# Kernel tuning notes

Measured on AMD Instinct MI355X. Metric: run time of the kernel, lower is better.

The kernel has to match this reference:

```python
import jax, jax.numpy as jnp
import numpy as np

B, T, M, S = 16384, 128, 4, 12  # num_series, timesteps, measurements, states


def setup_inputs() -> dict:
    key = jax.random.key(0)
    ks = jax.random.split(key, 7)
    inp = jax.random.normal(ks[0], (B, T, M), dtype=jnp.float32)
    # stable transition matrix near identity
    F = jnp.eye(S, dtype=jnp.float32) + 0.05 * jax.random.normal(ks[1], (S, S), dtype=jnp.float32) / np.float32(np.sqrt(S))
    H = jax.random.normal(ks[2], (M, S), dtype=jnp.float32) / np.float32(np.sqrt(S))
    Aq = 0.1 * jax.random.normal(ks[3], (S, S), dtype=jnp.float32)
    Q = Aq @ Aq.T + 1e-3 * jnp.eye(S, dtype=jnp.float32)  # PSD process noise
    Ar = 0.1 * jax.random.normal(ks[4], (M, M), dtype=jnp.float32)
    R = Ar @ Ar.T + 1e-3 * jnp.eye(M, dtype=jnp.float32)  # PSD measurement noise
    m0 = jax.random.normal(ks[5], (B, S, 1), dtype=jnp.float32)
    Ap = 0.1 * jax.random.normal(ks[6], (B, S, S), dtype=jnp.float32)
    P0 = jnp.einsum('bij,bkj->bik', Ap, Ap) + 1e-2 * jnp.eye(S, dtype=jnp.float32)
    return {"inp": inp, "F": F, "H": H, "Q": Q, "R": R, "m0": m0, "P0": P0}


def _kalman_forward(inp, F, H, Q, R, m0, P0):
    I_S = jnp.eye(S, dtype=inp.dtype)
    # t = -1 step of the original loop: one predict from the initial state
    m = jnp.einsum('ij,bjk->bik', F, m0)                      # [B,S,1]
    P = jnp.einsum('ij,bjk,lk->bil', F, P0, F) + Q            # [B,S,S]

    def step(carry, obs_t):
        m, P = carry  # one-step-ahead prior at time t
        y = jnp.einsum('ms,bsk->bmk', H, m)                   # predicted measurement [B,M,1]
        # --- kf_update ---
        resid = obs_t - y[..., 0]                             # [B,M]
        Sm = jnp.einsum('ms,bst,nt->bmn', H, P, H) + R        # innovation cov [B,M,M]
        Sinv = jnp.linalg.inv(Sm)
        K = jnp.einsum('bst,mt,bmn->bsn', P, H, Sinv)         # Kalman gain [B,S,M]
        m_f = m + jnp.einsum('bsm,bm->bs', K, resid)[..., None]
        ImKH = I_S - jnp.einsum('bsm,mt->bst', K, H)
        # Joseph stabilized covariance update
        P_f = (jnp.einsum('bij,bjk,blk->bil', ImKH, P, ImKH)
               + jnp.einsum('bim,mn,bjn->bij', K, R, K))
        # --- kf_predict for next timestep ---
        m_n = jnp.einsum('ij,bjk->bik', F, m_f)
        P_n = jnp.einsum('ij,bjk,lk->bil', F, P_f, F) + Q
        return (m_n, P_n), y

    _, ys = jax.lax.scan(step, (m, P), jnp.swapaxes(inp, 0, 1))  # ys: [T,B,M,1]
    # original forward does torch.cat(predicted_measurements, 0) -> [T*B, M, 1]
    return ys.reshape(T * B, M, 1)


def reference(inp, F, H, Q, R, m0, P0):
    return _kalman_forward(inp, F, H, Q, R, m0, P0)
```

## Files before the change

### kernel.cpp

```cpp
#include <hip/hip_runtime.h>

#define BN 16384
#define TT 128
#define MM 4
#define SS 12
#define BLOCK 64
#define NSER (BLOCK / 4)
#define TSTRIDE 145


template<int CTRL>
__device__ __forceinline__ float dpp32(float v) {
    union { int i; float f; } u, o;
    u.f = v;
    o.i = __builtin_amdgcn_update_dpp(0, u.i, CTRL, 0xF, 0xF, true);
    return o.f;
}
template<int CTRL>
__device__ __forceinline__ double dpp64(double v) {
    union { double d; int i[2]; } u, o;
    u.d = v;
    o.i[0] = __builtin_amdgcn_update_dpp(0, u.i[0], CTRL, 0xF, 0xF, true);
    o.i[1] = __builtin_amdgcn_update_dpp(0, u.i[1], CTRL, 0xF, 0xF, true);
    return o.d;
}
__device__ __forceinline__ double qsum(double v) {
    v += dpp64<0xB1>(v);
    v += dpp64<0x4E>(v);
    return v;
}

__global__ __launch_bounds__(BLOCK, 1) void kf_kernel(
    const float* __restrict__ inp,
    const float* __restrict__ Fm,
    const float* __restrict__ Hm,
    const float* __restrict__ Qm,
    const float* __restrict__ Rm,
    const float* __restrict__ m0p,
    const float* __restrict__ P0p,
    float* __restrict__ outp)
{
    __shared__ double Fd[SS * SS];
    __shared__ double Hd[MM * SS];
    __shared__ double Qd[SS * SS];
    __shared__ double Rd[MM * MM];
    __shared__ double tb[NSER * TSTRIDE];

    const int tid  = threadIdx.x;
    const int gid  = blockIdx.x * BLOCK + tid;
    const int b    = gid >> 2;
    const int c    = gid & 3;
    const int sb   = tid >> 2;
    const int col0 = 3 * c;

    for (int i = tid; i < SS * SS; i += BLOCK) {
        Fd[i] = (double)Fm[i];
        Qd[i] = (double)Qm[i];
    }
    if (tid < MM * SS) Hd[tid] = (double)Hm[tid];
    if (tid < MM * MM) Rd[tid] = (double)Rm[tid];

    double P[SS][3];
#pragma unroll
    for (int s = 0; s < SS; ++s)
#pragma unroll
        for (int jj = 0; jj < 3; ++jj)
            P[s][jj] = (double)P0p[b * SS * SS + s * SS + col0 + jj];

    double mtmp[SS];
#pragma unroll
    for (int s = 0; s < SS; ++s) mtmp[s] = (double)m0p[b * SS + s];

    const float* op = inp + b * (TT * MM) + c;
    float obn = op[0];
    double* tser = &tb[sb * TSTRIDE];

    __syncthreads();

#pragma unroll
    for (int i = 0; i < SS; ++i) {
        double fr[SS];
#pragma unroll
        for (int s = 0; s < SS; ++s) fr[s] = Fd[i * SS + s];
        double u0 = 0.0, u1 = 0.0, u2 = 0.0;
#pragma unroll
        for (int s = 0; s < SS; ++s) {
            u0 += fr[s] * P[s][0];
            u1 += fr[s] * P[s][1];
            u2 += fr[s] * P[s][2];
        }
        tser[i * SS + col0 + 0] = u0;
        tser[i * SS + col0 + 1] = u1;
        tser[i * SS + col0 + 2] = u2;
    }
    double pmv[3];
#pragma unroll
    for (int jj = 0; jj < 3; ++jj) {
        double a = 0.0;
#pragma unroll
        for (int s = 0; s < SS; ++s) a += Fd[(col0 + jj) * SS + s] * mtmp[s];
        pmv[jj] = a;
    }
    __builtin_amdgcn_wave_barrier();
#pragma unroll
    for (int h = 0; h < 2; ++h) {
        double Ur[3][6];
#pragma unroll
        for (int jj = 0; jj < 3; ++jj)
#pragma unroll
            for (int kk = 0; kk < 6; ++kk)
                Ur[jj][kk] = tser[(col0 + jj) * SS + h * 6 + kk];
#pragma unroll
        for (int s = 0; s < SS; ++s) {
            double fr6[6];
#pragma unroll
            for (int kk = 0; kk < 6; ++kk) fr6[kk] = Fd[s * SS + h * 6 + kk];
            double p0 = (h == 0) ? Qd[s * SS + col0 + 0] : P[s][0];
            double p1 = (h == 0) ? Qd[s * SS + col0 + 1] : P[s][1];
            double p2 = (h == 0) ? Qd[s * SS + col0 + 2] : P[s][2];
#pragma unroll
            for (int kk = 0; kk < 6; ++kk) {
                p0 += Ur[0][kk] * fr6[kk];
                p1 += Ur[1][kk] * fr6[kk];
                p2 += Ur[2][kk] * fr6[kk];
            }
            P[s][0] = p0; P[s][1] = p1; P[s][2] = p2;
        }
    }
    double mvf[SS];
    mvf[0]  = dpp64<0x00>(pmv[0]);  mvf[1]  = dpp64<0x00>(pmv[1]);  mvf[2]  = dpp64<0x00>(pmv[2]);
    mvf[3]  = dpp64<0x55>(pmv[0]);  mvf[4]  = dpp64<0x55>(pmv[1]);  mvf[5]  = dpp64<0x55>(pmv[2]);
    mvf[6]  = dpp64<0xAA>(pmv[0]);  mvf[7]  = dpp64<0xAA>(pmv[1]);  mvf[8]  = dpp64<0xAA>(pmv[2]);
    mvf[9]  = dpp64<0xFF>(pmv[0]);  mvf[10] = dpp64<0xFF>(pmv[1]);  mvf[11] = dpp64<0xFF>(pmv[2]);

#pragma unroll 1
    for (int t = 0; t < TT; ++t) {
        __builtin_amdgcn_wave_barrier();

#pragma unroll
        for (int i = 0; i < SS; ++i) {
            double fr[SS];
#pragma unroll
            for (int s = 0; s < SS; ++s) fr[s] = Fd[i * SS + s];
            double u0 = 0.0, u1 = 0.0, u2 = 0.0;
#pragma unroll
            for (int s = 0; s < SS; ++s) {
                u0 += fr[s] * P[s][0];
                u1 += fr[s] * P[s][1];
                u2 += fr[s] * P[s][2];
            }
            tser[i * SS + col0 + 0] = u0;
            tser[i * SS + col0 + 1] = u1;
            tser[i * SS + col0 + 2] = u2;
        }

        double fmv[3];
#pragma unroll
        for (int jj = 0; jj < 3; ++jj) {
            double a = 0.0;
#pragma unroll
            for (int s = 0; s < SS; ++s) a += Fd[(col0 + jj) * SS + s] * mvf[s];
            fmv[jj] = a;
        }

        double y[MM];
#pragma unroll
        for (int n = 0; n < MM; ++n) {
            double py = Hd[n * SS + col0 + 0] * mvf[col0 + 0]
                      + Hd[n * SS + col0 + 1] * mvf[col0 + 1]
                      + Hd[n * SS + col0 + 2] * mvf[col0 + 2];
            y[n] = qsum(py);
        }
        double ysel = (c & 2) ? ((c & 1) ? y[3] : y[2]) : ((c & 1) ? y[1] : y[0]);
        outp[t * (BN * MM) + b * MM + c] = (float)ysel;

        float obc = obn;
        if (t + 1 < TT) obn = op[(t + 1) * MM];

        double r[MM];
        r[0] = (double)dpp32<0x00>(obc) - y[0];
        r[1] = (double)dpp32<0x55>(obc) - y[1];
        r[2] = (double)dpp32<0xAA>(obc) - y[2];
        r[3] = (double)dpp32<0xFF>(obc) - y[3];

        double HPl[MM][3];
#pragma unroll
        for (int n = 0; n < MM; ++n) {
            double h0 = 0.0, h1 = 0.0, h2 = 0.0;
#pragma unroll
            for (int s = 0; s < SS; ++s) {
                double hv = Hd[n * SS + s];
                h0 += hv * P[s][0]; h1 += hv * P[s][1]; h2 += hv * P[s][2];
            }
            HPl[n][0] = h0; HPl[n][1] = h1; HPl[n][2] = h2;
        }

        double Su[10];
        {
            int u = 0;
#pragma unroll
            for (int n = 0; n < MM; ++n)
#pragma unroll
                for (int t2 = 0; t2 < MM; ++t2) {
                    if (t2 < n) continue;
                    double acc = HPl[n][0] * Hd[t2 * SS + col0 + 0]
                               + HPl[n][1] * Hd[t2 * SS + col0 + 1]
                               + HPl[n][2] * Hd[t2 * SS + col0 + 2];
                    Su[u] = qsum(acc) + Rd[n * MM + t2];
                    ++u;
                }
        }
        double s00 = Su[0], s01 = Su[1], s02 = Su[2], s03 = Su[3];
        double s11 = Su[4], s12 = Su[5], s13 = Su[6];
        double s22 = Su[7], s23 = Su[8], s33 = Su[9];

        __builtin_amdgcn_wave_barrier();

#pragma unroll
        for (int h = 0; h < 2; ++h) {
            double Ur[3][6];
#pragma unroll
            for (int jj = 0; jj < 3; ++jj)
#pragma unroll
                for (int kk = 0; kk < 6; ++kk)
                    Ur[jj][kk] = tser[(col0 + jj) * SS + h * 6 + kk];
#pragma unroll
            for (int s = 0; s < SS; ++s) {
                double fr6[6];
#pragma unroll
                for (int kk = 0; kk < 6; ++kk) fr6[kk] = Fd[s * SS + h * 6 + kk];
                double p0 = (h == 0) ? Qd[s * SS + col0 + 0] : P[s][0];
                double p1 = (h == 0) ? Qd[s * SS + col0 + 1] : P[s][1];
                double p2 = (h == 0) ? Qd[s * SS + col0 + 2] : P[s][2];
#pragma unroll
                for (int kk = 0; kk < 6; ++kk) {
                    p0 += Ur[0][kk] * fr6[kk];
                    p1 += Ur[1][kk] * fr6[kk];
                    p2 += Ur[2][kk] * fr6[kk];
                }
                P[s][0] = p0; P[s][1] = p1; P[s][2] = p2;
            }
        }

        double Vl[MM][3];
        {
            double h00 = dpp64<0x00>(HPl[0][0]), h01 = dpp64<0x00>(HPl[0][1]), h02 = dpp64<0x00>(HPl[0][2]);
            double h10 = dpp64<0x00>(HPl[1][0]), h11 = dpp64<0x00>(HPl[1][1]), h12 = dpp64<0x00>(HPl[1][2]);
            double h20 = dpp64<0x00>(HPl[2][0]), h21 = dpp64<0x00>(HPl[2][1]), h22 = dpp64<0x00>(HPl[2][2]);
            double h30 = dpp64<0x00>(HPl[3][0]), h31 = dpp64<0x00>(HPl[3][1]), h32 = dpp64<0x00>(HPl[3][2]);
#pragma unroll
            for (int jj = 0; jj < 3; ++jj) {
                double f0 = Fd[(col0 + jj) * SS + 0], f1 = Fd[(col0 + jj) * SS + 1], f2 = Fd[(col0 + jj) * SS + 2];
                Vl[0][jj] = h00 * f0 + h01 * f1 + h02 * f2;
                Vl[1][jj] = h10 * f0 + h11 * f1 + h12 * f2;
                Vl[2][jj] = h20 * f0 + h21 * f1 + h22 * f2;
                Vl[3][jj] = h30 * f0 + h31 * f1 + h32 * f2;
            }
        }
        {
            double h00 = dpp64<0x55>(HPl[0][0]), h01 = dpp64<0x55>(HPl[0][1]), h02 = dpp64<0x55>(HPl[0][2]);
            double h10 = dpp64<0x55>(HPl[1][0]), h11 = dpp64<0x55>(HPl[1][1]), h12 = dpp64<0x55>(HPl[1][2]);
            double h20 = dpp64<0x55>(HPl[2][0]), h21 = dpp64<0x55>(HPl[2][1]), h22 = dpp64<0x55>(HPl[2][2]);
            double h30 = dpp64<0x55>(HPl[3][0]), h31 = dpp64<0x55>(HPl[3][1]), h32 = dpp64<0x55>(HPl[3][2]);
#pragma unroll
            for (int jj = 0; jj < 3; ++jj) {
                double f0 = Fd[(col0 + jj) * SS + 3], f1 = Fd[(col0 + jj) * SS + 4], f2 = Fd[(col0 + jj) * SS + 5];
                Vl[0][jj] += h00 * f0 + h01 * f1 + h02 * f2;
                Vl[1][jj] += h10 * f0 + h11 * f1 + h12 * f2;
                Vl[2][jj] += h20 * f0 + h21 * f1 + h22 * f2;
                Vl[3][jj] += h30 * f0 + h31 * f1 + h32 * f2;
            }
        }
        {
            double h00 = dpp64<0xAA>(HPl[0][0]), h01 = dpp64<0xAA>(HPl[0][1]), h02 = dpp64<0xAA>(HPl[0][2]);
            double h10 = dpp64<0xAA>(HPl[1][0]), h11 = dpp64<0xAA>(HPl[1][1]), h12 = dpp64<0xAA>(HPl[1][2]);
            double h20 = dpp64<0xAA>(HPl[2][0]), h21 = dpp64<0xAA>(HPl[2][1]), h22 = dpp64<0xAA>(HPl[2][2]);
            double h30 = dpp64<0xAA>(HPl[3][0]), h31 = dpp64<0xAA>(HPl[3][1]), h32 = dpp64<0xAA>(HPl[3][2]);
#pragma unroll
            for (int jj = 0; jj < 3; ++jj) {
                double f0 = Fd[(col0 + jj) * SS + 6], f1 = Fd[(col0 + jj) * SS + 7], f2 = Fd[(col0 + jj) * SS + 8];
                Vl[0][jj] += h00 * f0 + h01 * f1 + h02 * f2;
                Vl[1][jj] += h10 * f0 + h11 * f1 + h12 * f2;
                Vl[2][jj] += h20 * f0 + h21 * f1 + h22 * f2;
                Vl[3][jj] += h30 * f0 + h31 * f1 + h32 * f2;
            }
        }
        {
            double h00 = dpp64<0xFF>(HPl[0][0]), h01 = dpp64<0xFF>(HPl[0][1]), h02 = dpp64<0xFF>(HPl[0][2]);
            double h10 = dpp64<0xFF>(HPl[1][0]), h11 = dpp64<0xFF>(HPl[1][1]), h12 = dpp64<0xFF>(HPl[1][2]);
            double h20 = dpp64<0xFF>(HPl[2][0]), h21 = dpp64<0xFF>(HPl[2][1]), h22 = dpp64<0xFF>(HPl[2][2]);
            double h30 = dpp64<0xFF>(HPl[3][0]), h31 = dpp64<0xFF>(HPl[3][1]), h32 = dpp64<0xFF>(HPl[3][2]);
#pragma unroll
            for (int jj = 0; jj < 3; ++jj) {
                double f0 = Fd[(col0 + jj) * SS + 9], f1 = Fd[(col0 + jj) * SS + 10], f2 = Fd[(col0 + jj) * SS + 11];
                Vl[0][jj] += h00 * f0 + h01 * f1 + h02 * f2;
                Vl[1][jj] += h10 * f0 + h11 * f1 + h12 * f2;
                Vl[2][jj] += h20 * f0 + h21 * f1 + h22 * f2;
                Vl[3][jj] += h30 * f0 + h31 * f1 + h32 * f2;
            }
        }

        double ra   = 1.0 / (s00 * s11 - s01 * s01);
        double ai00 = s11 * ra, ai01 = -s01 * ra, ai11 = s00 * ra;
        double w00 = ai00 * s02 + ai01 * s12;
        double w01 = ai00 * s03 + ai01 * s13;
        double w10 = ai01 * s02 + ai11 * s12;
        double w11 = ai01 * s03 + ai11 * s13;
        double e00 = s22 - (s02 * w00 + s12 * w10);
        double e01 = s23 - (s02 * w01 + s12 * w11);
        double e11 = s33 - (s03 * w01 + s13 * w11);
        double rmm = 1.0 / (e00 * e11 - e01 * e01);
        double q22 = e11 * rmm, q23 = -e01 * rmm, q33 = e00 * rmm;
        double x00 = w00 * q22 + w01 * q23;
        double x01 = w00 * q23 + w01 * q33;
        double x10 = w10 * q22 + w11 * q23;
        double x11 = w10 * q23 + w11 * q33;
        double q00 = ai00 + x00 * w00 + x01 * w01;
        double q01 = ai01 + x00 * w10 + x01 * w11;
        double q11 = ai11 + x10 * w10 + x11 * w11;
        double Qi[MM][MM] = {
            { q00,  q01,  -x00, -x01 },
            { q01,  q11,  -x10, -x11 },
            { -x00, -x10,  q22,  q23 },
            { -x01, -x11,  q23,  q33 }
        };

        double z0 = Qi[0][0] * r[0] + Qi[0][1] * r[1] + Qi[0][2] * r[2] + Qi[0][3] * r[3];
        double z1 = Qi[1][0] * r[0] + Qi[1][1] * r[1] + Qi[1][2] * r[2] + Qi[1][3] * r[3];
        double z2 = Qi[2][0] * r[0] + Qi[2][1] * r[1] + Qi[2][2] * r[2] + Qi[2][3] * r[3];
        double z3 = Qi[3][0] * r[0] + Qi[3][1] * r[1] + Qi[3][2] * r[2] + Qi[3][3] * r[3];

        double G2[MM][3];
#pragma unroll
        for (int n = 0; n < MM; ++n)
#pragma unroll
            for (int jj = 0; jj < 3; ++jj)
                G2[n][jj] = Qi[n][0] * Vl[0][jj] + Qi[n][1] * Vl[1][jj]
                          + Qi[n][2] * Vl[2][jj] + Qi[n][3] * Vl[3][jj];

        {
            double v00 = dpp64<0x00>(Vl[0][0]), v01 = dpp64<0x00>(Vl[0][1]), v02 = dpp64<0x00>(Vl[0][2]);
            double v10 = dpp64<0x00>(Vl[1][0]), v11 = dpp64<0x00>(Vl[1][1]), v12 = dpp64<0x00>(Vl[1][2]);
            double v20 = dpp64<0x00>(Vl[2][0]), v21 = dpp64<0x00>(Vl[2][1]), v22 = dpp64<0x00>(Vl[2][2]);
            double v30 = dpp64<0x00>(Vl[3][0]), v31 = dpp64<0x00>(Vl[3][1]), v32 = dpp64<0x00>(Vl[3][2]);
#pragma unroll
            for (int jj = 0; jj < 3; ++jj) {
                P[0][jj] -= v00 * G2[0][jj] + v10 * G2[1][jj] + v20 * G2[2][jj] + v30 * G2[3][jj];
                P[1][jj] -= v01 * G2[0][jj] + v11 * G2[1][jj] + v21 * G2[2][jj] + v31 * G2[3][jj];
                P[2][jj] -= v02 * G2[0][jj] + v12 * G2[1][jj] + v22 * G2[2][jj] + v32 * G2[3][jj];
            }
        }
        {
            double v00 = dpp64<0x55>(Vl[0][0]), v01 = dpp64<0x55>(Vl[0][1]), v02 = dpp64<0x55>(Vl[0][2]);
            double v10 = dpp64<0x55>(Vl[1][0]), v11 = dpp64<0x55>(Vl[1][1]), v12 = dpp64<0x55>(Vl[1][2]);
            double v20 = dpp64<0x55>(Vl[2][0]), v21 = dpp64<0x55>(Vl[2][1]), v22 = dpp64<0x55>(Vl[2][2]);
            double v30 = dpp64<0x55>(Vl[3][0]), v31 = dpp64<0x55>(Vl[3][1]), v32 = dpp64<0x55>(Vl[3][2]);
#pragma unroll
            for (int jj = 0; jj < 3; ++jj) {
                P[3][jj] -= v00 * G2[0][jj] + v10 * G2[1][jj] + v20 * G2[2][jj] + v30 * G2[3][jj];
                P[4][jj] -= v01 * G2[0][jj] + v11 * G2[1][jj] + v21 * G2[2][jj] + v31 * G2[3][jj];
                P[5][jj] -= v02 * G2[0][jj] + v12 * G2[1][jj] + v22 * G2[2][jj] + v32 * G2[3][jj];
            }
        }
        {
            double v00 = dpp64<0xAA>(Vl[0][0]), v01 = dpp64<0xAA>(Vl[0][1]), v02 = dpp64<0xAA>(Vl[0][2]);
            double v10 = dpp64<0xAA>(Vl[1][0]), v11 = dpp64<0xAA>(Vl[1][1]), v12 = dpp64<0xAA>(Vl[1][2]);
            double v20 = dpp64<0xAA>(Vl[2][0]), v21 = dpp64<0xAA>(Vl[2][1]), v22 = dpp64<0xAA>(Vl[2][2]);
            double v30 = dpp64<0xAA>(Vl[3][0]), v31 = dpp64<0xAA>(Vl[3][1]), v32 = dpp64<0xAA>(Vl[3][2]);
#pragma unroll
            for (int jj = 0; jj < 3; ++jj) {
                P[6][jj] -= v00 * G2[0][jj] + v10 * G2[1][jj] + v20 * G2[2][jj] + v30 * G2[3][jj];
                P[7][jj] -= v01 * G2[0][jj] + v11 * G2[1][jj] + v21 * G2[2][jj] + v31 * G2[3][jj];
                P[8][jj] -= v02 * G2[0][jj] + v12 * G2[1][jj] + v22 * G2[2][jj] + v32 * G2[3][jj];
            }
        }
        {
            double v00 = dpp64<0xFF>(Vl[0][0]), v01 = dpp64<0xFF>(Vl[0][1]), v02 = dpp64<0xFF>(Vl[0][2]);
            double v10 = dpp64<0xFF>(Vl[1][0]), v11 = dpp64<0xFF>(Vl[1][1]), v12 = dpp64<0xFF>(Vl[1][2]);
            double v20 = dpp64<0xFF>(Vl[2][0]), v21 = dpp64<0xFF>(Vl[2][1]), v22 = dpp64<0xFF>(Vl[2][2]);
            double v30 = dpp64<0xFF>(Vl[3][0]), v31 = dpp64<0xFF>(Vl[3][1]), v32 = dpp64<0xFF>(Vl[3][2]);
#pragma unroll
            for (int jj = 0; jj < 3; ++jj) {
                P[9][jj]  -= v00 * G2[0][jj] + v10 * G2[1][jj] + v20 * G2[2][jj] + v30 * G2[3][jj];
                P[10][jj] -= v01 * G2[0][jj] + v11 * G2[1][jj] + v21 * G2[2][jj] + v31 * G2[3][jj];
                P[11][jj] -= v02 * G2[0][jj] + v12 * G2[1][jj] + v22 * G2[2][jj] + v32 * G2[3][jj];
            }
        }

        double mvn[3];
#pragma unroll
        for (int jj = 0; jj < 3; ++jj)
            mvn[jj] = fmv[jj] + Vl[0][jj] * z0 + Vl[1][jj] * z1
                    + Vl[2][jj] * z2 + Vl[3][jj] * z3;

        mvf[0]  = dpp64<0x00>(mvn[0]);  mvf[1]  = dpp64<0x00>(mvn[1]);  mvf[2]  = dpp64<0x00>(mvn[2]);
        mvf[3]  = dpp64<0x55>(mvn[0]);  mvf[4]  = dpp64<0x55>(mvn[1]);  mvf[5]  = dpp64<0x55>(mvn[2]);
        mvf[6]  = dpp64<0xAA>(mvn[0]);  mvf[7]  = dpp64<0xAA>(mvn[1]);  mvf[8]  = dpp64<0xAA>(mvn[2]);
        mvf[9]  = dpp64<0xFF>(mvn[0]);  mvf[10] = dpp64<0xFF>(mvn[1]);  mvf[11] = dpp64<0xFF>(mvn[2]);
    }
}

extern "C" void kernel_launch(void* const* d_in, const int* in_sizes, int n_in,
                              void* d_out, int out_size, void* d_ws, size_t ws_size,
                              hipStream_t stream) {
    const float* inp = (const float*)d_in[0];
    const float* F   = (const float*)d_in[1];
    const float* H   = (const float*)d_in[2];
    const float* Q   = (const float*)d_in[3];
    const float* R   = (const float*)d_in[4];
    const float* m0  = (const float*)d_in[5];
    const float* P0  = (const float*)d_in[6];
    float* out = (float*)d_out;

    dim3 grid((BN * MM) / BLOCK), block(BLOCK);
    hipLaunchKernelGGL(kf_kernel, grid, block, 0, stream,
                       inp, F, H, Q, R, m0, P0, out);
}
```

Baseline: 849.1 us.

## Interleave covariance predict chunks with the innovation-inverse chain using register pins

Measured after the change: 821.0 us. -3.3%, faster.

```diff
diff --git a/kernel.cpp b/kernel.cpp
--- a/kernel.cpp
+++ b/kernel.cpp
@@ -30,6 +30,15 @@
     return v;
 }
 
+#define PIN_P_LO() asm volatile("" : "+v"(P[0][0]),"+v"(P[0][1]),"+v"(P[0][2]), \
+    "+v"(P[1][0]),"+v"(P[1][1]),"+v"(P[1][2]),"+v"(P[2][0]),"+v"(P[2][1]),"+v"(P[2][2]), \
+    "+v"(P[3][0]),"+v"(P[3][1]),"+v"(P[3][2]),"+v"(P[4][0]),"+v"(P[4][1]),"+v"(P[4][2]), \
+    "+v"(P[5][0]),"+v"(P[5][1]),"+v"(P[5][2]))
+#define PIN_P_HI() asm volatile("" : "+v"(P[6][0]),"+v"(P[6][1]),"+v"(P[6][2]), \
+    "+v"(P[7][0]),"+v"(P[7][1]),"+v"(P[7][2]),"+v"(P[8][0]),"+v"(P[8][1]),"+v"(P[8][2]), \
+    "+v"(P[9][0]),"+v"(P[9][1]),"+v"(P[9][2]),"+v"(P[10][0]),"+v"(P[10][1]),"+v"(P[10][2]), \
+    "+v"(P[11][0]),"+v"(P[11][1]),"+v"(P[11][2]))
+
 __global__ __launch_bounds__(BLOCK, 1) void kf_kernel(
     const float* __restrict__ inp,
     const float* __restrict__ Fm,
@@ -127,6 +136,9 @@
             P[s][0] = p0; P[s][1] = p1; P[s][2] = p2;
         }
     }
+    double pml[3];
+#pragma unroll
+    for (int jj = 0; jj < 3; ++jj) pml[jj] = pmv[jj];
     double mvf[SS];
     mvf[0]  = dpp64<0x00>(pmv[0]);  mvf[1]  = dpp64<0x00>(pmv[1]);  mvf[2]  = dpp64<0x00>(pmv[2]);
     mvf[3]  = dpp64<0x55>(pmv[0]);  mvf[4]  = dpp64<0x55>(pmv[1]);  mvf[5]  = dpp64<0x55>(pmv[2]);
@@ -138,7 +150,7 @@
         __builtin_amdgcn_wave_barrier();
 
 #pragma unroll
-        for (int i = 0; i < SS; ++i) {
+        for (int i = 0; i < 6; ++i) {
             double fr[SS];
 #pragma unroll
             for (int s = 0; s < SS; ++s) fr[s] = Fd[i * SS + s];
@@ -154,35 +166,6 @@
             tser[i * SS + col0 + 2] = u2;
         }
 
-        double fmv[3];
-#pragma unroll
-        for (int jj = 0; jj < 3; ++jj) {
-            double a = 0.0;
-#pragma unroll
-            for (int s = 0; s < SS; ++s) a += Fd[(col0 + jj) * SS + s] * mvf[s];
-            fmv[jj] = a;
-        }
-
-        double y[MM];
-#pragma unroll
-        for (int n = 0; n < MM; ++n) {
-            double py = Hd[n * SS + col0 + 0] * mvf[col0 + 0]
-                      + Hd[n * SS + col0 + 1] * mvf[col0 + 1]
-                      + Hd[n * SS + col0 + 2] * mvf[col0 + 2];
-            y[n] = qsum(py);
-        }
-        double ysel = (c & 2) ? ((c & 1) ? y[3] : y[2]) : ((c & 1) ? y[1] : y[0]);
-        outp[t * (BN * MM) + b * MM + c] = (float)ysel;
-
-        float obc = obn;
-        if (t + 1 < TT) obn = op[(t + 1) * MM];
-
-        double r[MM];
-        r[0] = (double)dpp32<0x00>(obc) - y[0];
-        r[1] = (double)dpp32<0x55>(obc) - y[1];
-        r[2] = (double)dpp32<0xAA>(obc) - y[2];
-        r[3] = (double)dpp32<0xFF>(obc) - y[3];
-
         double HPl[MM][3];
 #pragma unroll
         for (int n = 0; n < MM; ++n) {
@@ -194,6 +177,25 @@
             }
             HPl[n][0] = h0; HPl[n][1] = h1; HPl[n][2] = h2;
         }
+
+        double y[MM];
+#pragma unroll
+        for (int n = 0; n < MM; ++n) {
+            double py = Hd[n * SS + col0 + 0] * pml[0]
+                      + Hd[n * SS + col0 + 1] * pml[1]
+                      + Hd[n * SS + col0 + 2] * pml[2];
+            y[n] = qsum(py);
+        }
+        double ysel = (c & 2) ? ((c & 1) ? y[3] : y[2]) : ((c & 1) ? y[1] : y[0]);
+        outp[t * (BN * MM) + b * MM + c] = (float)ysel;
+
+        float obc = obn;
+        if (t + 1 < TT) obn = op[(t + 1) * MM];
+
+        double r0v = (double)dpp32<0x00>(obc) - y[0];
+        double r1v = (double)dpp32<0x55>(obc) - y[1];
+        double r2v = (double)dpp32<0xAA>(obc) - y[2];
+        double r3v = (double)dpp32<0xFF>(obc) - y[3];
 
         double Su[10];
         {
@@ -214,90 +216,66 @@
         double s11 = Su[4], s12 = Su[5], s13 = Su[6];
         double s22 = Su[7], s23 = Su[8], s33 = Su[9];
 
+        double fmv[3];
+#pragma unroll
+        for (int jj = 0; jj < 3; ++jj) {
+            double a = 0.0;
+#pragma unroll
+            for (int s = 0; s < SS; ++s) a += Fd[(col0 + jj) * SS + s] * mvf[s];
+            fmv[jj] = a;
+        }
+
+        asm volatile("" : "+v"(HPl[0][0]),"+v"(HPl[0][1]),"+v"(HPl[0][2]),
+                          "+v"(HPl[1][0]),"+v"(HPl[1][1]),"+v"(HPl[1][2]),
+                          "+v"(HPl[2][0]),"+v"(HPl[2][1]),"+v"(HPl[2][2]),
+                          "+v"(HPl[3][0]),"+v"(HPl[3][1]),"+v"(HPl[3][2]),
+                          "+v"(s00),"+v"(s01),"+v"(s02),"+v"(s03),"+v"(s11),
+                          "+v"(s12),"+v"(s13),"+v"(s22),"+v"(s23),"+v"(s33),
+                          "+v"(r0v),"+v"(r1v),"+v"(r2v),"+v"(r3v),
+                          "+v"(fmv[0]),"+v"(fmv[1]),"+v"(fmv[2]));
+        PIN_P_LO(); PIN_P_HI();
+
+#pragma unroll
+        for (int i = 6; i < SS; ++i) {
+            double fr[SS];
+#pragma unroll
+            for (int s = 0; s < SS; ++s) fr[s] = Fd[i * SS + s];
+            double u0 = 0.0, u1 = 0.0, u2 = 0.0;
+#pragma unroll
+            for (int s = 0; s < SS; ++s) {
+                u0 += fr[s] * P[s][0];
+                u1 += fr[s] * P[s][1];
+                u2 += fr[s] * P[s][2];
+            }
+            tser[i * SS + col0 + 0] = u0;
+            tser[i * SS + col0 + 1] = u1;
+            tser[i * SS + col0 + 2] = u2;
+        }
+
         __builtin_amdgcn_wave_barrier();
 
-#pragma unroll
-        for (int h = 0; h < 2; ++h) {
-            double Ur[3][6];
-#pragma unroll
-            for (int jj = 0; jj < 3; ++jj)
-#pragma unroll
-                for (int kk = 0; kk < 6; ++kk)
-                    Ur[jj][kk] = tser[(col0 + jj) * SS + h * 6 + kk];
-#pragma unroll
-            for (int s = 0; s < SS; ++s) {
-                double fr6[6];
-#pragma unroll
-                for (int kk = 0; kk < 6; ++kk) fr6[kk] = Fd[s * SS + h * 6 + kk];
-                double p0 = (h == 0) ? Qd[s * SS + col0 + 0] : P[s][0];
-                double p1 = (h == 0) ? Qd[s * SS + col0 + 1] : P[s][1];
-                double p2 = (h == 0) ? Qd[s * SS + col0 + 2] : P[s][2];
-#pragma unroll
-                for (int kk = 0; kk < 6; ++kk) {
-                    p0 += Ur[0][kk] * fr6[kk];
-                    p1 += Ur[1][kk] * fr6[kk];
-                    p2 += Ur[2][kk] * fr6[kk];
-                }
-                P[s][0] = p0; P[s][1] = p1; P[s][2] = p2;
-            }
-        }
-
-        double Vl[MM][3];
-        {
-            double h00 = dpp64<0x00>(HPl[0][0]), h01 = dpp64<0x00>(HPl[0][1]), h02 = dpp64<0x00>(HPl[0][2]);
-            double h10 = dpp64<0x00>(HPl[1][0]), h11 = dpp64<0x00>(HPl[1][1]), h12 = dpp64<0x00>(HPl[1][2]);
-            double h20 = dpp64<0x00>(HPl[2][0]), h21 = dpp64<0x00>(HPl[2][1]), h22 = dpp64<0x00>(HPl[2][2]);
-            double h30 = dpp64<0x00>(HPl[3][0]), h31 = dpp64<0x00>(HPl[3][1]), h32 = dpp64<0x00>(HPl[3][2]);
-#pragma unroll
-            for (int jj = 0; jj < 3; ++jj) {
-                double f0 = Fd[(col0 + jj) * SS + 0], f1 = Fd[(col0 + jj) * SS + 1], f2 = Fd[(col0 + jj) * SS + 2];
-                Vl[0][jj] = h00 * f0 + h01 * f1 + h02 * f2;
-                Vl[1][jj] = h10 * f0 + h11 * f1 + h12 * f2;
-                Vl[2][jj] = h20 * f0 + h21 * f1 + h22 * f2;
-                Vl[3][jj] = h30 * f0 + h31 * f1 + h32 * f2;
-            }
-        }
-        {
-            double h00 = dpp64<0x55>(HPl[0][0]), h01 = dpp64<0x55>(HPl[0][1]), h02 = dpp64<0x55>(HPl[0][2]);
-            double h10 = dpp64<0x55>(HPl[1][0]), h11 = dpp64<0x55>(HPl[1][1]), h12 = dpp64<0x55>(HPl[1][2]);
-            double h20 = dpp64<0x55>(HPl[2][0]), h21 = dpp64<0x55>(HPl[2][1]), h22 = dpp64<0x55>(HPl[2][2]);
-            double h30 = dpp64<0x55>(HPl[3][0]), h31 = dpp64<0x55>(HPl[3][1]), h32 = dpp64<0x55>(HPl[3][2]);
-#pragma unroll
-            for (int jj = 0; jj < 3; ++jj) {
-                double f0 = Fd[(col0 + jj) * SS + 3], f1 = Fd[(col0 + jj) * SS + 4], f2 = Fd[(col0 + jj) * SS + 5];
-                Vl[0][jj] += h00 * f0 + h01 * f1 + h02 * f2;
-                Vl[1][jj] += h10 * f0 + h11 * f1 + h12 * f2;
-                Vl[2][jj] += h20 * f0 + h21 * f1 + h22 * f2;
-                Vl[3][jj] += h30 * f0 + h31 * f1 + h32 * f2;
-            }
-        }
-        {
-            double h00 = dpp64<0xAA>(HPl[0][0]), h01 = dpp64<0xAA>(HPl[0][1]), h02 = dpp64<0xAA>(HPl[0][2]);
-            double h10 = dpp64<0xAA>(HPl[1][0]), h11 = dpp64<0xAA>(HPl[1][1]), h12 = dpp64<0xAA>(HPl[1][2]);
-            double h20 = dpp64<0xAA>(HPl[2][0]), h21 = dpp64<0xAA>(HPl[2][1]), h22 = dpp64<0xAA>(HPl[2][2]);
-            double h30 = dpp64<0xAA>(HPl[3][0]), h31 = dpp64<0xAA>(HPl[3][1]), h32 = dpp64<0xAA>(HPl[3][2]);
-#pragma unroll
-            for (int jj = 0; jj < 3; ++jj) {
-                double f0 = Fd[(col0 + jj) * SS + 6], f1 = Fd[(col0 + jj) * SS + 7], f2 = Fd[(col0 + jj) * SS + 8];
-                Vl[0][jj] += h00 * f0 + h01 * f1 + h02 * f2;
-                Vl[1][jj] += h10 * f0 + h11 * f1 + h12 * f2;
-                Vl[2][jj] += h20 * f0 + h21 * f1 + h22 * f2;
-                Vl[3][jj] += h30 * f0 + h31 * f1 + h32 * f2;
-            }
-        }
-        {
-            double h00 = dpp64<0xFF>(HPl[0][0]), h01 = dpp64<0xFF>(HPl[0][1]), h02 = dpp64<0xFF>(HPl[0][2]);
-            double h10 = dpp64<0xFF>(HPl[1][0]), h11 = dpp64<0xFF>(HPl[1][1]), h12 = dpp64<0xFF>(HPl[1][2]);
-            double h20 = dpp64<0xFF>(HPl[2][0]), h21 = dpp64<0xFF>(HPl[2][1]), h22 = dpp64<0xFF>(HPl[2][2]);
-            double h30 = dpp64<0xFF>(HPl[3][0]), h31 = dpp64<0xFF>(HPl[3][1]), h32 = dpp64<0xFF>(HPl[3][2]);
-#pragma unroll
-            for (int jj = 0; jj < 3; ++jj) {
-                double f0 = Fd[(col0 + jj) * SS + 9], f1 = Fd[(col0 + jj) * SS + 10], f2 = Fd[(col0 + jj) * SS + 11];
-                Vl[0][jj] += h00 * f0 + h01 * f1 + h02 * f2;
-                Vl[1][jj] += h10 * f0 + h11 * f1 + h12 * f2;
-                Vl[2][jj] += h20 * f0 + h21 * f1 + h22 * f2;
-                Vl[3][jj] += h30 * f0 + h31 * f1 + h32 * f2;
-            }
+        double Ur0[3][6];
+#pragma unroll
+        for (int jj = 0; jj < 3; ++jj)
+#pragma unroll
+            for (int kk = 0; kk < 6; ++kk)
+                Ur0[jj][kk] = tser[(col0 + jj) * SS + kk];
+
+#pragma unroll
+        for (int s = 0; s < 6; ++s) {
+            double fr6[6];
+#pragma unroll
+            for (int kk = 0; kk < 6; ++kk) fr6[kk] = Fd[s * SS + kk];
+            double p0 = Qd[s * SS + col0 + 0];
+            double p1 = Qd[s * SS + col0 + 1];
+            double p2 = Qd[s * SS + col0 + 2];
+#pragma unroll
+            for (int kk = 0; kk < 6; ++kk) {
+                p0 += Ur0[0][kk] * fr6[kk];
+                p1 += Ur0[1][kk] * fr6[kk];
+                p2 += Ur0[2][kk] * fr6[kk];
+            }
+            P[s][0] = p0; P[s][1] = p1; P[s][2] = p2;
         }
 
         double ra   = 1.0 / (s00 * s11 - s01 * s01);
@@ -306,11 +284,57 @@
         double w01 = ai00 * s03 + ai01 * s13;
         double w10 = ai01 * s02 + ai11 * s12;
         double w11 = ai01 * s03 + ai11 * s13;
+        asm volatile("" : "+v"(w00),"+v"(w01),"+v"(w10),"+v"(w11),
+                          "+v"(ai00),"+v"(ai01),"+v"(ai11));
+        PIN_P_HI();
+
+#pragma unroll
+        for (int s = 6; s < SS; ++s) {
+            double fr6[6];
+#pragma unroll
+            for (int kk = 0; kk < 6; ++kk) fr6[kk] = Fd[s * SS + kk];
+            double p0 = Qd[s * SS + col0 + 0];
+            double p1 = Qd[s * SS + col0 + 1];
+            double p2 = Qd[s * SS + col0 + 2];
+#pragma unroll
+            for (int kk = 0; kk < 6; ++kk) {
+                p0 += Ur0[0][kk] * fr6[kk];
+                p1 += Ur0[1][kk] * fr6[kk];
+                p2 += Ur0[2][kk] * fr6[kk];
+            }
+            P[s][0] = p0; P[s][1] = p1; P[s][2] = p2;
+        }
+
         double e00 = s22 - (s02 * w00 + s12 * w10);
         double e01 = s23 - (s02 * w01 + s12 * w11);
         double e11 = s33 - (s03 * w01 + s13 * w11);
         double rmm = 1.0 / (e00 * e11 - e01 * e01);
         double q22 = e11 * rmm, q23 = -e01 * rmm, q33 = e00 * rmm;
+        asm volatile("" : "+v"(q22),"+v"(q23),"+v"(q33));
+        PIN_P_LO();
+
+        double Ur1[3][6];
+#pragma unroll
+        for (int jj = 0; jj < 3; ++jj)
+#pragma unroll
+            for (int kk = 0; kk < 6; ++kk)
+                Ur1[jj][kk] = tser[(col0 + jj) * SS + 6 + kk];
+
+#pragma unroll
+        for (int s = 0; s < 6; ++s) {
+            double fr6[6];
+#pragma unroll
+            for (int kk = 0; kk < 6; ++kk) fr6[kk] = Fd[s * SS + 6 + kk];
+            double p0 = P[s][0], p1 = P[s][1], p2 = P[s][2];
+#pragma unroll
+            for (int kk = 0; kk < 6; ++kk) {
+                p0 += Ur1[0][kk] * fr6[kk];
+                p1 += Ur1[1][kk] * fr6[kk];
+                p2 += Ur1[2][kk] * fr6[kk];
+            }
+            P[s][0] = p0; P[s][1] = p1; P[s][2] = p2;
+        }
+
         double x00 = w00 * q22 + w01 * q23;
         double x01 = w00 * q23 + w01 * q33;
         double x10 = w10 * q22 + w11 * q23;
@@ -318,6 +342,30 @@
         double q00 = ai00 + x00 * w00 + x01 * w01;
         double q01 = ai01 + x00 * w10 + x01 * w11;
         double q11 = ai11 + x10 * w10 + x11 * w11;
+        double z0 =  q00 * r0v + q01 * r1v - x00 * r2v - x01 * r3v;
+        double z1 =  q01 * r0v + q11 * r1v - x10 * r2v - x11 * r3v;
+        double z2 = -x00 * r0v - x10 * r1v + q22 * r2v + q23 * r3v;
+        double z3 = -x01 * r0v - x11 * r1v + q23 * r2v + q33 * r3v;
+        asm volatile("" : "+v"(z0),"+v"(z1),"+v"(z2),"+v"(z3),
+                          "+v"(x00),"+v"(x01),"+v"(x10),"+v"(x11),
+                          "+v"(q00),"+v"(q01),"+v"(q11));
+        PIN_P_HI();
+
+#pragma unroll
+        for (int s = 6; s < SS; ++s) {
+            double fr6[6];
+#pragma unroll
+            for (int kk = 0; kk < 6; ++kk) fr6[kk] = Fd[s * SS + 6 + kk];
+            double p0 = P[s][0], p1 = P[s][1], p2 = P[s][2];
+#pragma unroll
+            for (int kk = 0; kk < 6; ++kk) {
+                p0 += Ur1[0][kk] * fr6[kk];
+                p1 += Ur1[1][kk] * fr6[kk];
+                p2 += Ur1[2][kk] * fr6[kk];
+            }
+            P[s][0] = p0; P[s][1] = p1; P[s][2] = p2;
+        }
+
         double Qi[MM][MM] = {
             { q00,  q01,  -x00, -x01 },
             { q01,  q11,  -x10, -x11 },
@@ -325,10 +373,63 @@
             { -x01, -x11,  q23,  q33 }
         };
 
-        double z0 = Qi[0][0] * r[0] + Qi[0][1] * r[1] + Qi[0][2] * r[2] + Qi[0][3] * r[3];
-        double z1 = Qi[1][0] * r[0] + Qi[1][1] * r[1] + Qi[1][2] * r[2] + Qi[1][3] * r[3];
-        double z2 = Qi[2][0] * r[0] + Qi[2][1] * r[1] + Qi[2][2] * r[2] + Qi[2][3] * r[3];
-        double z3 = Qi[3][0] * r[0] + Qi[3][1] * r[1] + Qi[3][2] * r[2] + Qi[3][3] * r[3];
+        double Vl[MM][3];
+        {
+            double h00 = dpp64<0x00>(HPl[0][0]), h01 = dpp64<0x00>(HPl[0][1]), h02 = dpp64<0x00>(HPl[0][2]);
+            double h10 = dpp64<0x00>(HPl[1][0]), h11 = dpp64<0x00>(HPl[1][1]), h12 = dpp64<0x00>(HPl[1][2]);
+            double h20 = dpp64<0x00>(HPl[2][0]), h21 = dpp64<0x00>(HPl[2][1]), h22 = dpp64<0x00>(HPl[2][2]);
+            double h30 = dpp64<0x00>(HPl[3][0]), h31 = dpp64<0x00>(HPl[3][1]), h32 = dpp64<0x00>(HPl[3][2]);
+#pragma unroll
+            for (int jj = 0; jj < 3; ++jj) {
+                double f0 = Fd[(col0 + jj) * SS + 0], f1 = Fd[(col0 + jj) * SS + 1], f2 = Fd[(col0 + jj) * SS + 2];
+                Vl[0][jj] = h00 * f0 + h01 * f1 + h02 * f2;
+                Vl[1][jj] = h10 * f0 + h11 * f1 + h12 * f2;
+                Vl[2][jj] = h20 * f0 + h21 * f1 + h22 * f2;
+                Vl[3][jj] = h30 * f0 + h31 * f1 + h32 * f2;
+            }
+        }
+        {
+            double h00 = dpp64<0x55>(HPl[0][0]), h01 = dpp64<0x55>(HPl[0][1]), h02 = dpp64<0x55>(HPl[0][2]);
+            double h10 = dpp64<0x55>(HPl[1][0]), h11 = dpp64<0x55>(HPl[1][1]), h12 = dpp64<0x55>(HPl[1][2]);
+            double h20 = dpp64<0x55>(HPl[2][0]), h21 = dpp64<0x55>(HPl[2][1]), h22 = dpp64<0x55>(HPl[2][2]);
+            double h30 = dpp64<0x55>(HPl[3][0]), h31 = dpp64<0x55>(HPl[3][1]), h32 = dpp64<0x55>(HPl[3][2]);
+#pragma unroll
+            for (int jj = 0; jj < 3; ++jj) {
+                double f0 = Fd[(col0 + jj) * SS + 3], f1 = Fd[(col0 + jj) * SS + 4], f2 = Fd[(col0 + jj) * SS + 5];
+                Vl[0][jj] += h00 * f0 + h01 * f1 + h02 * f2;
+                Vl[1][jj] += h10 * f0 + h11 * f1 + h12 * f2;
+                Vl[2][jj] += h20 * f0 + h21 * f1 + h22 * f2;
+                Vl[3][jj] += h30 * f0 + h31 * f1 + h32 * f2;
+            }
+        }
+        {
+            double h00 = dpp64<0xAA>(HPl[0][0]), h01 = dpp64<0xAA>(HPl[0][1]), h02 = dpp64<0xAA>(HPl[0][2]);
+            double h10 = dpp64<0xAA>(HPl[1][0]), h11 = dpp64<0xAA>(HPl[1][1]), h12 = dpp64<0xAA>(HPl[1][2]);
+            double h20 = dpp64<0xAA>(HPl[2][0]), h21 = dpp64<0xAA>(HPl[2][1]), h22 = dpp64<0xAA>(HPl[2][2]);
+            double h30 = dpp64<0xAA>(HPl[3][0]), h31 = dpp64<0xAA>(HPl[3][1]), h32 = dpp64<0xAA>(HPl[3][2]);
+#pragma unroll
+            for (int jj = 0; jj < 3; ++jj) {
+                double f0 = Fd[(col0 + jj) * SS + 6], f1 = Fd[(col0 + jj) * SS + 7], f2 = Fd[(col0 + jj) * SS + 8];
+                Vl[0][jj] += h00 * f0 + h01 * f1 + h02 * f2;
+                Vl[1][jj] += h10 * f0 + h11 * f1 + h12 * f2;
+                Vl[2][jj] += h20 * f0 + h21 * f1 + h22 * f2;
+                Vl[3][jj] += h30 * f0 + h31 * f1 + h32 * f2;
+            }
+        }
+        {
+            double h00 = dpp64<0xFF>(HPl[0][0]), h01 = dpp64<0xFF>(HPl[0][1]), h02 = dpp64<0xFF>(HPl[0][2]);
+            double h10 = dpp64<0xFF>(HPl[1][0]), h11 = dpp64<0xFF>(HPl[1][1]), h12 = dpp64<0xFF>(HPl[1][2]);
+            double h20 = dpp64<0xFF>(HPl[2][0]), h21 = dpp64<0xFF>(HPl[2][1]), h22 = dpp64<0xFF>(HPl[2][2]);
+            double h30 = dpp64<0xFF>(HPl[3][0]), h31 = dpp64<0xFF>(HPl[3][1]), h32 = dpp64<0xFF>(HPl[3][2]);
+#pragma unroll
+            for (int jj = 0; jj < 3; ++jj) {
+                double f0 = Fd[(col0 + jj) * SS + 9], f1 = Fd[(col0 + jj) * SS + 10], f2 = Fd[(col0 + jj) * SS + 11];
+                Vl[0][jj] += h00 * f0 + h01 * f1 + h02 * f2;
+                Vl[1][jj] += h10 * f0 + h11 * f1 + h12 * f2;
+                Vl[2][jj] += h20 * f0 + h21 * f1 + h22 * f2;
+                Vl[3][jj] += h30 * f0 + h31 * f1 + h32 * f2;
+            }
+        }
 
         double G2[MM][3];
 #pragma unroll
@@ -393,6 +494,7 @@
             mvn[jj] = fmv[jj] + Vl[0][jj] * z0 + Vl[1][jj] * z1
                     + Vl[2][jj] * z2 + Vl[3][jj] * z3;
 
+        pml[0] = mvn[0]; pml[1] = mvn[1]; pml[2] = mvn[2];
         mvf[0]  = dpp64<0x00>(mvn[0]);  mvf[1]  = dpp64<0x00>(mvn[1]);  mvf[2]  = dpp64<0x00>(mvn[2]);
         mvf[3]  = dpp64<0x55>(mvn[0]);  mvf[4]  = dpp64<0x55>(mvn[1]);  mvf[5]  = dpp64<0x55>(mvn[2]);
         mvf[6]  = dpp64<0xAA>(mvn[0]);  mvf[7]  = dpp64<0xAA>(mvn[1]);  mvf[8]  = dpp64<0xAA>(mvn[2]);
```
